# Optimization experiments

Measured on AMD Instinct MI355X. Metric: run time of the kernel, lower is better.

## Reference

```python
import jax, jax.numpy as jnp
import numpy as np

N_NODES = 100000
N_EDGES = 1600000
IN_FEATS = 128
ATTN_FEATS = 64
NUM_HEADS = 4
OUT_FEATS = 32
NEG_SLOPE = 0.2


def setup_inputs() -> dict:
    key = jax.random.key(0)
    ks = jax.random.split(key, 8)
    feat = jax.random.normal(ks[0], (N_NODES, IN_FEATS), dtype=jnp.float32)
    attn_feat = jax.random.normal(ks[1], (N_NODES, ATTN_FEATS), dtype=jnp.float32)
    # fc: ReparameterizedLinear(in=IN_FEATS, out=OUT*HEADS, bias=False), raw weight
    fc_weight = jax.random.normal(ks[2], (NUM_HEADS * OUT_FEATS, IN_FEATS), dtype=jnp.float32) * (1.0 / np.sqrt(IN_FEATS))
    fc_attn_weight = jax.random.normal(ks[3], (NUM_HEADS * OUT_FEATS, ATTN_FEATS), dtype=jnp.float32) * (1.0 / np.sqrt(ATTN_FEATS))
    attn_l = jax.random.normal(ks[4], (1, NUM_HEADS, OUT_FEATS), dtype=jnp.float32)
    attn_r = jax.random.normal(ks[5], (1, NUM_HEADS, OUT_FEATS), dtype=jnp.float32)
    src = jax.random.randint(ks[6], (N_EDGES,), 0, N_NODES, dtype=jnp.int32)
    dst = jax.random.randint(ks[7], (N_EDGES,), 0, N_NODES, dtype=jnp.int32)
    return {"feat": feat, "attn_feat": attn_feat, "fc_weight": fc_weight,
            "fc_attn_weight": fc_attn_weight, "attn_l": attn_l, "attn_r": attn_r,
            "src": src, "dst": dst}


def reference(feat, attn_feat, fc_weight, fc_attn_weight, attn_l, attn_r, src, dst):
    H, F = NUM_HEADS, OUT_FEATS
    N = feat.shape[0]
    # ReparameterizedLinear with reparam_method='ReLU', is_increasing=True:
    # effective weight is relu(raw weight) -> nonnegative, monotone increasing.
    w = jax.nn.relu(fc_weight)                                  # [H*F, in]
    feat_src = (feat @ w.T).reshape(N, H, F)                    # [N,H,F]
    attn_proj = (attn_feat @ fc_attn_weight.T).reshape(N, H, F)  # [N,H,F]
    el = jnp.sum(attn_proj * attn_l, axis=-1)                   # [N,H]
    er = jnp.sum(attn_proj * attn_r, axis=-1)                   # [N,H]
    # u_add_v + leaky_relu on edges
    e = jax.nn.leaky_relu(el[src] + er[dst], NEG_SLOPE)          # [E,H]
    # edge_softmax: segment softmax keyed by destination node
    m = jax.ops.segment_max(e, dst, num_segments=N)              # [N,H]
    ex = jnp.exp(e - m[dst])                                     # [E,H]
    denom = jax.ops.segment_sum(ex, dst, num_segments=N)         # [N,H]
    a = ex / denom[dst]                                          # [E,H]
    # u_mul_e + sum aggregation
    msg = feat_src[src] * a[:, :, None]                          # [E,H,F]
    rst = jax.ops.segment_sum(msg, dst, num_segments=N)          # [N,H,F]
    return rst
```

## Files before the change

kernel.cpp:

```cpp
#include <hip/hip_runtime.h>
#include <math.h>

#define N_NODES   100000
#define N_EDGES   1600000
#define IN_FEATS  128
#define ATTN_FEATS 64
#define NUM_HEADS 4
#define OUT_FEATS 32
#define HF        128
#define NEG_SLOPE 0.2f
#define SLOT_CAP  64

#define BKN       128
#define NB        ((N_NODES + BKN - 1) / BKN)
#define C_BLOCKS  196
#define C_EDGES   8192
#define PROJ_BLOCKS ((N_NODES / 32 + 3) / 4)
#define ELER_NPB    64
#define ELER_BLOCKS ((N_NODES + ELER_NPB - 1) / ELER_NPB)
#define P1_BLOCKS (C_BLOCKS * 13)

typedef __bf16 bf16x8 __attribute__((ext_vector_type(8)));
typedef float  f32x4  __attribute__((ext_vector_type(4)));

__device__ __forceinline__ ushort f2b(float f) {
  uint u = __float_as_uint(f);
  return (ushort)((u + 0x7FFFu + ((u >> 16) & 1u)) >> 16);
}

__global__ __launch_bounds__(256) void phase1_kernel(
    const float*  __restrict__ feat,
    const float*  __restrict__ fc_w,
    ushort* __restrict__ feat_src,
    const float* __restrict__ attn_feat,
    const float* __restrict__ fc_aw,
    const float* __restrict__ attn_l,
    const float* __restrict__ attn_r,
    float* __restrict__ el, float* __restrict__ er,
    const int* __restrict__ src, const int* __restrict__ dst,
    uint* __restrict__ ebuf,
    uint* __restrict__ dir) {
  int q = blockIdx.x / 13, role = blockIdx.x % 13;
  int t = threadIdx.x;

  if (role == 0) {
    __shared__ int lcnt[NB];
    __shared__ int lbase[NB];
    int cb = q;
    size_t ebase = (size_t)cb * C_EDGES;
    for (int i = t; i < NB; i += 256) lcnt[i] = 0;
    __syncthreads();
    #pragma unroll 4
    for (int r = 0; r < C_EDGES / 256; ++r) {
      size_t e = ebase + r * 256 + t;
      if (e < N_EDGES) atomicAdd(&lcnt[dst[e] >> 7], 1);
    }
    __syncthreads();
    if (t < 64) {
      int carry = 0;
      for (int c = 0; c < (NB + 63) / 64; ++c) {
        int idx = c * 64 + t;
        int v = (idx < NB) ? lcnt[idx] : 0;
        int incl = v;
        #pragma unroll
        for (int d = 1; d < 64; d <<= 1) {
          int x = __shfl_up(incl, d);
          if (t >= d) incl += x;
        }
        int tot = __shfl(incl, 63);
        if (idx < NB) lbase[idx] = carry + incl - v;
        carry += tot;
      }
    }
    __syncthreads();
    for (int i = t; i < NB; i += 256)
      dir[(size_t)i * C_BLOCKS + cb] = ((uint)lbase[i] << 8) | (uint)min(lcnt[i], 255);
    __syncthreads();
    #pragma unroll 4
    for (int r = 0; r < C_EDGES / 256; ++r) {
      size_t e = ebase + r * 256 + t;
      if (e < N_EDGES) {
        int dv = dst[e];
        int rk = atomicAdd(&lbase[dv >> 7], 1);
        ebuf[ebase + rk] = ((uint)(dv & 127) << 20) | (uint)src[e];
      }
    }
    return;
  }

  if (role <= 4) {
    int pb = q * 4 + (role - 1);
    if (pb >= PROJ_BLOCKS) return;
    int wave = t >> 6;
    int lane = t & 63;
    int mbase = (pb * 4 + wave) * 32;
    if (mbase >= N_NODES) return;
    int r  = lane & 15;
    int kg = lane >> 4;

    f32x4 acc[2][8];
    #pragma unroll
    for (int i = 0; i < 2; ++i)
      #pragma unroll
      for (int j = 0; j < 8; ++j) acc[i][j] = (f32x4)0.f;

    #pragma unroll
    for (int ks = 0; ks < 4; ++ks) {
      int kbase = ks * 32 + kg * 8;
      bf16x8 a[2];
      #pragma unroll
      for (int i = 0; i < 2; ++i) {
        const float* fp = &feat[(size_t)(mbase + i * 16 + r) * IN_FEATS + kbase];
        float4 f0 = *(const float4*)fp;
        float4 f1 = *(const float4*)(fp + 4);
        a[i][0] = (__bf16)f0.x; a[i][1] = (__bf16)f0.y;
        a[i][2] = (__bf16)f0.z; a[i][3] = (__bf16)f0.w;
        a[i][4] = (__bf16)f1.x; a[i][5] = (__bf16)f1.y;
        a[i][6] = (__bf16)f1.z; a[i][7] = (__bf16)f1.w;
      }
      #pragma unroll
      for (int nt = 0; nt < 8; ++nt) {
        const float* wp = &fc_w[(size_t)(nt * 16 + r) * IN_FEATS + kbase];
        float4 w0 = *(const float4*)wp;
        float4 w1 = *(const float4*)(wp + 4);
        bf16x8 b;
        b[0] = (__bf16)fmaxf(w0.x, 0.f); b[1] = (__bf16)fmaxf(w0.y, 0.f);
        b[2] = (__bf16)fmaxf(w0.z, 0.f); b[3] = (__bf16)fmaxf(w0.w, 0.f);
        b[4] = (__bf16)fmaxf(w1.x, 0.f); b[5] = (__bf16)fmaxf(w1.y, 0.f);
        b[6] = (__bf16)fmaxf(w1.z, 0.f); b[7] = (__bf16)fmaxf(w1.w, 0.f);
        acc[0][nt] = __builtin_amdgcn_mfma_f32_16x16x32_bf16(a[0], b, acc[0][nt], 0, 0, 0);
        acc[1][nt] = __builtin_amdgcn_mfma_f32_16x16x32_bf16(a[1], b, acc[1][nt], 0, 0, 0);
      }
    }
    #pragma unroll
    for (int i = 0; i < 2; ++i)
      #pragma unroll
      for (int nt = 0; nt < 8; ++nt)
        #pragma unroll
        for (int qd = 0; qd < 4; ++qd) {
          int node = mbase + i * 16 + kg * 4 + qd;
          feat_src[(size_t)node * HF + nt * 16 + r] = f2b(acc[i][nt][qd]);
        }
    return;
  }

  {
    int eb = q * 8 + (role - 5);
    if (eb >= ELER_BLOCKS) return;
    __shared__ float af[ELER_NPB * 65];
    __shared__ float svl[NUM_HEADS * 65], svr[NUM_HEADS * 65];
    int nbase = eb * ELER_NPB;
    int nmax = min(ELER_NPB, N_NODES - nbase);
    {
      int h = t >> 6, k = t & 63;
      float sl = 0.f, sr = 0.f;
      #pragma unroll 8
      for (int f = 0; f < OUT_FEATS; ++f) {
        float w = fc_aw[(size_t)(h * OUT_FEATS + f) * ATTN_FEATS + k];
        sl = fmaf(w, attn_l[h * OUT_FEATS + f], sl);
        sr = fmaf(w, attn_r[h * OUT_FEATS + f], sr);
      }
      svl[h * 65 + k] = sl;
      svr[h * 65 + k] = sr;
    }
    for (int i = t; i < ELER_NPB * ATTN_FEATS / 4; i += 256) {
      int ni = i >> 4, kq = i & 15;
      if (ni < nmax) {
        const float4 g = *(const float4*)&attn_feat[(size_t)(nbase + ni) * ATTN_FEATS + kq * 4];
        af[ni * 65 + kq * 4 + 0] = g.x;
        af[ni * 65 + kq * 4 + 1] = g.y;
        af[ni * 65 + kq * 4 + 2] = g.z;
        af[ni * 65 + kq * 4 + 3] = g.w;
      }
    }
    __syncthreads();
    int n = t >> 2, h = t & 3;
    if (n < nmax) {
      float al = 0.f, ar = 0.f;
      #pragma unroll 8
      for (int k = 0; k < ATTN_FEATS; ++k) {
        float a = af[n * 65 + k];
        al = fmaf(a, svl[h * 65 + k], al);
        ar = fmaf(a, svr[h * 65 + k], ar);
      }
      el[(size_t)(nbase + n) * NUM_HEADS + h] = al;
      er[(size_t)(nbase + n) * NUM_HEADS + h] = ar;
    }
  }
}

__global__ __launch_bounds__(256) void compact_kernel(
    const uint* __restrict__ ebuf, const uint* __restrict__ dir,
    int* __restrict__ counts, int* __restrict__ es_slot) {
  __shared__ int lcnt[BKN];
  __shared__ uint sdir[C_BLOCKS];
  int b = blockIdx.x;
  int t = threadIdx.x;
  for (int i = t; i < BKN; i += 256) lcnt[i] = 0;
  if (t < C_BLOCKS) sdir[t] = dir[(size_t)b * C_BLOCKS + t];
  __syncthreads();
  if (t < C_BLOCKS) {
    uint dv = sdir[t];
    int cnt = dv & 255;
    uint start = (uint)t * C_EDGES + (dv >> 8);
    int nbase = b * BKN;
    for (int j = 0; j < cnt; ++j) {
      uint w = ebuf[start + j];
      int nl = w >> 20;
      int rk = atomicAdd(&lcnt[nl], 1);
      if (rk < SLOT_CAP)
        es_slot[(size_t)(nbase + nl) * SLOT_CAP + rk] = (int)(w & 0xFFFFF);
    }
  }
  __syncthreads();
  int nmax = min(BKN, N_NODES - b * BKN);
  for (int i = t; i < nmax; i += 256) counts[b * BKN + i] = lcnt[i];
}

__global__ __launch_bounds__(256) void aggregate_kernel(
    const int* __restrict__ counts, const int* __restrict__ es_slot,
    const float* __restrict__ el, const float* __restrict__ er,
    const ushort* __restrict__ feat_src, float* __restrict__ out) {
  int wv = threadIdx.x >> 6;
  int lane = threadIdx.x & 63;
  int d0 = blockIdx.x * 8 + wv * 2;
  int d1 = d0 + 1;
  int hA = lane & 3;
  int ceA = lane >> 2;
  int g  = lane >> 4;
  int c  = lane & 15;
  int hC = c >> 2;

  int cnt0 = min(counts[d0], SLOT_CAP);
  int cnt1 = min(counts[d1], SLOT_CAP);
  const int* row0 = &es_slot[(size_t)d0 * SLOT_CAP];
  const int* row1 = &es_slot[(size_t)d1 * SLOT_CAP];
  float er_h0 = er[(size_t)d0 * NUM_HEADS + hA];
  float er_h1 = er[(size_t)d1 * NUM_HEADS + hA];
  float s0 = 0.f, s1 = 0.f;
  float acc0[8], acc1[8];
  #pragma unroll
  for (int j = 0; j < 8; ++j) { acc0[j] = 0.f; acc1[j] = 0.f; }

  int cmax = max(cnt0, cnt1);
  for (int cb = 0; cb < cmax; cb += 16) {
    int cnum0 = min(16, cnt0 - cb);
    int cnum1 = min(16, cnt1 - cb);
    float p0 = 0.f, p1 = 0.f;
    int sidx0 = 0, sidx1 = 0;
    if (ceA < cnum0) sidx0 = row0[cb + ceA];
    if (ceA < cnum1) sidx1 = row1[cb + ceA];
    if (ceA < cnum0) {
      float ev = el[(size_t)sidx0 * NUM_HEADS + hA] + er_h0;
      ev = ev > 0.f ? ev : NEG_SLOPE * ev;
      p0 = __expf(ev);
    }
    if (ceA < cnum1) {
      float ev = el[(size_t)sidx1 * NUM_HEADS + hA] + er_h1;
      ev = ev > 0.f ? ev : NEG_SLOPE * ev;
      p1 = __expf(ev);
    }
    float ps0 = p0, ps1 = p1;
    #pragma unroll
    for (int dlt = 4; dlt < 64; dlt <<= 1) {
      ps0 += __shfl_xor(ps0, dlt);
      ps1 += __shfl_xor(ps1, dlt);
    }
    s0 += ps0;
    s1 += ps1;
    int ni0 = (cnum0 > 0) ? ((cnum0 + 3) >> 2) : 0;
    int ni1 = (cnum1 > 0) ? ((cnum1 + 3) >> 2) : 0;
    #pragma unroll
    for (int i = 0; i < 4; ++i) {
      int srcLane = 16 * i + 4 * g + hC;
      if (i < ni0) {
        float pb = __shfl(p0, srcLane);
        int   sb = __shfl(sidx0, srcLane);
        uint4 fv = *(const uint4*)&feat_src[(size_t)sb * HF + c * 8];
        acc0[0] = fmaf(pb, __uint_as_float(fv.x << 16), acc0[0]);
        acc0[1] = fmaf(pb, __uint_as_float(fv.x & 0xFFFF0000u), acc0[1]);
        acc0[2] = fmaf(pb, __uint_as_float(fv.y << 16), acc0[2]);
        acc0[3] = fmaf(pb, __uint_as_float(fv.y & 0xFFFF0000u), acc0[3]);
        acc0[4] = fmaf(pb, __uint_as_float(fv.z << 16), acc0[4]);
        acc0[5] = fmaf(pb, __uint_as_float(fv.z & 0xFFFF0000u), acc0[5]);
        acc0[6] = fmaf(pb, __uint_as_float(fv.w << 16), acc0[6]);
        acc0[7] = fmaf(pb, __uint_as_float(fv.w & 0xFFFF0000u), acc0[7]);
      }
      if (i < ni1) {
        float pb = __shfl(p1, srcLane);
        int   sb = __shfl(sidx1, srcLane);
        uint4 fv = *(const uint4*)&feat_src[(size_t)sb * HF + c * 8];
        acc1[0] = fmaf(pb, __uint_as_float(fv.x << 16), acc1[0]);
        acc1[1] = fmaf(pb, __uint_as_float(fv.x & 0xFFFF0000u), acc1[1]);
        acc1[2] = fmaf(pb, __uint_as_float(fv.y << 16), acc1[2]);
        acc1[3] = fmaf(pb, __uint_as_float(fv.y & 0xFFFF0000u), acc1[3]);
        acc1[4] = fmaf(pb, __uint_as_float(fv.z << 16), acc1[4]);
        acc1[5] = fmaf(pb, __uint_as_float(fv.z & 0xFFFF0000u), acc1[5]);
        acc1[6] = fmaf(pb, __uint_as_float(fv.w << 16), acc1[6]);
        acc1[7] = fmaf(pb, __uint_as_float(fv.w & 0xFFFF0000u), acc1[7]);
      }
    }
  }
  #pragma unroll
  for (int j = 0; j < 8; ++j) {
    acc0[j] += __shfl_xor(acc0[j], 16);
    acc0[j] += __shfl_xor(acc0[j], 32);
    acc1[j] += __shfl_xor(acc1[j], 16);
    acc1[j] += __shfl_xor(acc1[j], 32);
  }
  float sB0 = __shfl(s0, hC);
  float sB1 = __shfl(s1, hC);
  float inv0 = (sB0 > 0.f) ? 1.f / sB0 : 0.f;
  float inv1 = (sB1 > 0.f) ? 1.f / sB1 : 0.f;
  float2 o0 = {acc0[g * 2] * inv0, acc0[g * 2 + 1] * inv0};
  float2 o1 = {acc1[g * 2] * inv1, acc1[g * 2 + 1] * inv1};
  *(float2*)&out[(size_t)d0 * HF + c * 8 + g * 2] = o0;
  *(float2*)&out[(size_t)d1 * HF + c * 8 + g * 2] = o1;
}

extern "C" void kernel_launch(void* const* d_in, const int* in_sizes, int n_in,
                              void* d_out, int out_size, void* d_ws, size_t ws_size,
                              hipStream_t stream) {
  const float* feat      = (const float*)d_in[0];
  const float* attn_feat = (const float*)d_in[1];
  const float* fc_w      = (const float*)d_in[2];
  const float* fc_aw     = (const float*)d_in[3];
  const float* attn_l    = (const float*)d_in[4];
  const float* attn_r    = (const float*)d_in[5];
  const int*   src       = (const int*)d_in[6];
  const int*   dst       = (const int*)d_in[7];
  float* out = (float*)d_out;

  size_t off = 0;
  auto carve = [&](size_t bytes) -> void* {
    void* p = (char*)d_ws + off;
    off += (bytes + 255) & ~(size_t)255;
    return p;
  };
  float*  el       = (float*)carve((size_t)N_NODES * NUM_HEADS * 4);
  float*  er       = (float*)carve((size_t)N_NODES * NUM_HEADS * 4);
  ushort* feat_src = (ushort*)carve((size_t)N_NODES * HF * 2);
  int*    counts   = (int*)carve((size_t)N_NODES * 4);
  int*    es_slot  = (int*)carve((size_t)N_NODES * SLOT_CAP * 4);
  uint*   ebuf     = (uint*)carve((size_t)C_BLOCKS * C_EDGES * 4);
  uint*   dir      = (uint*)carve((size_t)NB * C_BLOCKS * 4);

  phase1_kernel<<<P1_BLOCKS, 256, 0, stream>>>(feat, fc_w, feat_src, attn_feat,
                                               fc_aw, attn_l, attn_r,
                                               el, er, src, dst, ebuf, dir);
  compact_kernel<<<NB, 256, 0, stream>>>(ebuf, dir, counts, es_slot);
  aggregate_kernel<<<N_NODES / 8, 256, 0, stream>>>(counts, es_slot, el, er, feat_src, out);
}
```

Before: 172.6 us.

## Rebalance phase1 block roles with smaller edge chunks and transposed directory

The edge-bucketing chunk shrinks from 8192 to 2560 edges, so 625 chunk blocks run instead of 196, and the per-chunk role mix in phase1 changes to one scatter, two projection and three el/er blocks. The scatter role now loads all dst and src values into registers up front, dropping the bounds checks and the second dst reload. The directory layout is transposed so the scatter writes contiguously, and the compact kernel loops over more than 256 chunks per node bucket. The aim is more parallelism and better load balance in phase1, at the cost of more directory entries and more serial chunk iterations per compact thread.

Result: faster. 161.2 us (-6.6%).

```diff
diff --git a/kernel.cpp b/kernel.cpp
--- a/kernel.cpp
+++ b/kernel.cpp
@@ -13,12 +13,13 @@
 
 #define BKN       128
 #define NB        ((N_NODES + BKN - 1) / BKN)
-#define C_BLOCKS  196
-#define C_EDGES   8192
+#define C_BLOCKS  625
+#define C_EDGES   2560
+#define SC_R      (C_EDGES / 256)
 #define PROJ_BLOCKS ((N_NODES / 32 + 3) / 4)
 #define ELER_NPB    64
 #define ELER_BLOCKS ((N_NODES + ELER_NPB - 1) / ELER_NPB)
-#define P1_BLOCKS (C_BLOCKS * 13)
+#define P1_BLOCKS (C_BLOCKS * 6)
 
 typedef __bf16 bf16x8 __attribute__((ext_vector_type(8)));
 typedef float  f32x4  __attribute__((ext_vector_type(4)));
@@ -40,7 +41,7 @@
     const int* __restrict__ src, const int* __restrict__ dst,
     uint* __restrict__ ebuf,
     uint* __restrict__ dir) {
-  int q = blockIdx.x / 13, role = blockIdx.x % 13;
+  int q = blockIdx.x / 6, role = blockIdx.x % 6;
   int t = threadIdx.x;
 
   if (role == 0) {
@@ -50,11 +51,11 @@
     size_t ebase = (size_t)cb * C_EDGES;
     for (int i = t; i < NB; i += 256) lcnt[i] = 0;
     __syncthreads();
-    #pragma unroll 4
-    for (int r = 0; r < C_EDGES / 256; ++r) {
-      size_t e = ebase + r * 256 + t;
-      if (e < N_EDGES) atomicAdd(&lcnt[dst[e] >> 7], 1);
-    }
+    int dv[SC_R];
+    #pragma unroll
+    for (int r = 0; r < SC_R; ++r) dv[r] = dst[ebase + r * 256 + t];
+    #pragma unroll
+    for (int r = 0; r < SC_R; ++r) atomicAdd(&lcnt[dv[r] >> 7], 1);
     __syncthreads();
     if (t < 64) {
       int carry = 0;
@@ -74,22 +75,21 @@
     }
     __syncthreads();
     for (int i = t; i < NB; i += 256)
-      dir[(size_t)i * C_BLOCKS + cb] = ((uint)lbase[i] << 8) | (uint)min(lcnt[i], 255);
-    __syncthreads();
-    #pragma unroll 4
-    for (int r = 0; r < C_EDGES / 256; ++r) {
-      size_t e = ebase + r * 256 + t;
-      if (e < N_EDGES) {
-        int dv = dst[e];
-        int rk = atomicAdd(&lbase[dv >> 7], 1);
-        ebuf[ebase + rk] = ((uint)(dv & 127) << 20) | (uint)src[e];
-      }
-    }
+      dir[(size_t)cb * NB + i] = ((uint)lbase[i] << 8) | (uint)min(lcnt[i], 255);
+    __syncthreads();
+    int sv[SC_R], rk[SC_R];
+    #pragma unroll
+    for (int r = 0; r < SC_R; ++r) sv[r] = src[ebase + r * 256 + t];
+    #pragma unroll
+    for (int r = 0; r < SC_R; ++r) rk[r] = atomicAdd(&lbase[dv[r] >> 7], 1);
+    #pragma unroll
+    for (int r = 0; r < SC_R; ++r)
+      ebuf[ebase + rk[r]] = ((uint)(dv[r] & 127) << 20) | (uint)sv[r];
     return;
   }
 
-  if (role <= 4) {
-    int pb = q * 4 + (role - 1);
+  if (role <= 2) {
+    int pb = q * 2 + (role - 1);
     if (pb >= PROJ_BLOCKS) return;
     int wave = t >> 6;
     int lane = t & 63;
@@ -145,7 +145,7 @@
   }
 
   {
-    int eb = q * 8 + (role - 5);
+    int eb = q * 3 + (role - 3);
     if (eb >= ELER_BLOCKS) return;
     __shared__ float af[ELER_NPB * 65];
     __shared__ float svl[NUM_HEADS * 65], svr[NUM_HEADS * 65];
@@ -197,13 +197,13 @@
   int b = blockIdx.x;
   int t = threadIdx.x;
   for (int i = t; i < BKN; i += 256) lcnt[i] = 0;
-  if (t < C_BLOCKS) sdir[t] = dir[(size_t)b * C_BLOCKS + t];
+  for (int i = t; i < C_BLOCKS; i += 256) sdir[i] = dir[(size_t)i * NB + b];
   __syncthreads();
-  if (t < C_BLOCKS) {
-    uint dv = sdir[t];
+  int nbase = b * BKN;
+  for (int s = t; s < C_BLOCKS; s += 256) {
+    uint dv = sdir[s];
     int cnt = dv & 255;
-    uint start = (uint)t * C_EDGES + (dv >> 8);
-    int nbase = b * BKN;
+    uint start = (uint)s * C_EDGES + (dv >> 8);
     for (int j = 0; j < cnt; ++j) {
       uint w = ebuf[start + j];
       int nl = w >> 20;
@@ -343,7 +343,7 @@
   int*    counts   = (int*)carve((size_t)N_NODES * 4);
   int*    es_slot  = (int*)carve((size_t)N_NODES * SLOT_CAP * 4);
   uint*   ebuf     = (uint*)carve((size_t)C_BLOCKS * C_EDGES * 4);
-  uint*   dir      = (uint*)carve((size_t)NB * C_BLOCKS * 4);
+  uint*   dir      = (uint*)carve((size_t)C_BLOCKS * NB * 4);
 
   phase1_kernel<<<P1_BLOCKS, 256, 0, stream>>>(feat, fc_w, feat_src, attn_feat,
                                                fc_aw, attn_l, attn_r,
```
